# Kernel tuning notes

Measured on AMD Instinct MI355X. Metric: run time of the kernel, lower is better.

## Reference

```python
import jax, jax.numpy as jnp
import numpy as np

# NF4 codebook (QLoRA): 16 quantile values of a standard normal, normalized to [-1, 1]
NF4_TABLE = jnp.array([
    -1.0, -0.6961928009986877, -0.5250730514526367, -0.39491748809814453,
    -0.28444138169288635, -0.18477343022823334, -0.09105003625154495, 0.0,
    0.07958029955625534, 0.16093020141124725, 0.24611230194568634,
    0.33791524171829224, 0.44070982933044434, 0.5626170039176941,
    0.7229568362236328, 1.0], dtype=jnp.float32)

IN_DIM = 4096
OUT_DIM = 4096
RANK = 16
ALPHA = 32.0
BLOCK = 64  # NF4 quantization block size along the flattened weight


def setup_inputs() -> dict:
    key = jax.random.key(0)
    k1, k2, k3, k4, k5 = jax.random.split(key, 5)
    x = jax.random.normal(k1, (4, 2048, IN_DIM), dtype=jnp.float32)
    # 4-bit codes into NF4_TABLE, stored unpacked as int32
    w_codes = jax.random.randint(k2, (OUT_DIM, IN_DIM), 0, 16, dtype=jnp.int32)
    # per-block absmax scales (positive)
    w_scales = jax.random.uniform(k3, (OUT_DIM, IN_DIM // BLOCK), dtype=jnp.float32) * 0.02 + 1e-3
    # lora_a: kaiming-uniform-ish scale; lora_b: nonzero for testability (original inits to zeros)
    lora_a = jax.random.normal(k4, (RANK, IN_DIM), dtype=jnp.float32) * (1.0 / np.sqrt(IN_DIM))
    lora_b = jax.random.normal(k5, (OUT_DIM, RANK), dtype=jnp.float32) * 0.01
    return {"x": x, "w_codes": w_codes, "w_scales": w_scales, "lora_a": lora_a, "lora_b": lora_b}


def _dequant_nf4(w_codes, w_scales):
    # codes [O, I] -> dequantized weight [O, I]
    w = NF4_TABLE[w_codes]                                   # [O, I]
    w = w.reshape(OUT_DIM, IN_DIM // BLOCK, BLOCK) * w_scales[:, :, None]
    return w.reshape(OUT_DIM, IN_DIM)


def reference(x, w_codes, w_scales, lora_a, lora_b):
    # base: frozen NF4 linear (dequantize then matmul), no bias
    w = _dequant_nf4(w_codes, w_scales)                      # [O, I]
    base = jnp.einsum('bsi,oi->bso', x, w)                   # [B, S, O]
    # LoRA path: dropout p=0.0 -> identity; scale alpha / rank
    ax = jnp.einsum('bsi,ri->bsr', x, lora_a)                # [B, S, r]
    lora = jnp.einsum('bsr,or->bso', ax, lora_b)             # [B, S, O]
    return base + (ALPHA / RANK) * lora
```

## Files before the change

### kernel.cpp

```cpp
#include <hip/hip_runtime.h>
#include <hip/hip_bf16.h>


#define IN_DIM  4096
#define OUT_DIM 4096
#define RANK    16
#define M_TOK   8192
#define LORA_SCALE 2.0f

typedef __bf16 bf16_t;
typedef bf16_t bf16x8 __attribute__((ext_vector_type(8)));
typedef float  f32x4  __attribute__((ext_vector_type(4)));

__device__ __constant__ float NF4_TAB[16] = {
    -1.0f, -0.6961928009986877f, -0.5250730514526367f, -0.39491748809814453f,
    -0.28444138169288635f, -0.18477343022823334f, -0.09105003625154495f, 0.0f,
    0.07958029955625534f, 0.16093020141124725f, 0.24611230194568634f,
    0.33791524171829224f, 0.44070982933044434f, 0.5626170039176941f,
    0.7229568362236328f, 1.0f};

__global__ __launch_bounds__(256) void prep_w(
    const int* __restrict__ codes,
    const float* __restrict__ scales,
    const float* __restrict__ la,
    const float* __restrict__ lb,
    bf16_t* __restrict__ W)
{
    __shared__ float nf4s[16];
    __shared__ float lbs[16];
    const int o = blockIdx.x;
    const int tid = threadIdx.x;
    if (tid < 16) {
        nf4s[tid] = NF4_TAB[tid];
        lbs[tid]  = lb[o * RANK + tid] * LORA_SCALE;
    }
    __syncthreads();

    #pragma unroll
    for (int it = 0; it < 2; ++it) {
        const int i0 = (it * 256 + tid) * 8;
        const size_t base = (size_t)o * IN_DIM + i0;
        int4 c0 = *(const int4*)(codes + base);
        int4 c1 = *(const int4*)(codes + base + 4);
        const float sc = scales[o * (IN_DIM / 64) + (i0 >> 6)];
        float w[8];
        w[0] = nf4s[c0.x] * sc; w[1] = nf4s[c0.y] * sc;
        w[2] = nf4s[c0.z] * sc; w[3] = nf4s[c0.w] * sc;
        w[4] = nf4s[c1.x] * sc; w[5] = nf4s[c1.y] * sc;
        w[6] = nf4s[c1.z] * sc; w[7] = nf4s[c1.w] * sc;
        #pragma unroll
        for (int r = 0; r < RANK; ++r) {
            const float b = lbs[r];
            float4 a0 = *(const float4*)(la + r * IN_DIM + i0);
            float4 a1 = *(const float4*)(la + r * IN_DIM + i0 + 4);
            w[0] += b * a0.x; w[1] += b * a0.y; w[2] += b * a0.z; w[3] += b * a0.w;
            w[4] += b * a1.x; w[5] += b * a1.y; w[6] += b * a1.z; w[7] += b * a1.w;
        }
        bf16x8 v;
        #pragma unroll
        for (int j = 0; j < 8; ++j) v[j] = (bf16_t)w[j];
        *(bf16x8*)(W + base) = v;
    }
}

__global__ __launch_bounds__(256) void cast_x(
    const float* __restrict__ x, bf16_t* __restrict__ y, int n8)
{
    const int stride = gridDim.x * blockDim.x;
    for (int i = blockIdx.x * blockDim.x + threadIdx.x; i < n8; i += stride) {
        const size_t e = (size_t)i * 8;
        float4 a = *(const float4*)(x + e);
        float4 b = *(const float4*)(x + e + 4);
        bf16x8 v;
        v[0] = (bf16_t)a.x; v[1] = (bf16_t)a.y; v[2] = (bf16_t)a.z; v[3] = (bf16_t)a.w;
        v[4] = (bf16_t)b.x; v[5] = (bf16_t)b.y; v[6] = (bf16_t)b.z; v[7] = (bf16_t)b.w;
        *(bf16x8*)(y + e) = v;
    }
}

#define BM 256
#define BN 256
#define BK 32
#define NT (IN_DIM / BK)

__global__ __launch_bounds__(512, 2) void gemm_bt(
    const bf16_t* __restrict__ A, const bf16_t* __restrict__ B,
    float* __restrict__ C)
{
    __shared__ bf16_t lds[3][2][BM * BK];

    const int tid  = threadIdx.x;
    const int wave = tid >> 6;
    const int lane = tid & 63;

    const int flat = blockIdx.y * gridDim.x + blockIdx.x;
    const int swz  = (flat & 7) * 64 + (flat >> 3);
    const int bx = swz & 15;
    const int by = swz >> 4;
    const int m0 = by * BM;
    const int n0 = bx * BN;

    const int wr = wave >> 2;
    const int wc = wave & 3;

    f32x4 acc[8][4];
    #pragma unroll
    for (int i = 0; i < 8; ++i)
        #pragma unroll
        for (int j = 0; j < 4; ++j) acc[i][j] = (f32x4)0.0f;

    const size_t KB = (size_t)IN_DIM * 2;

    int s_row[2], s_gc[2];
    #pragma unroll
    for (int p = 0; p < 2; ++p) {
        const int off = p * 8192 + tid * 16;
        s_row[p] = off >> 6;
        s_gc[p]  = ((off >> 4) & 3) ^ ((s_row[p] >> 1) & 3);
    }
    const char* gA = (const char*)A;
    const char* gB = (const char*)B;

    const int frow = lane & 15;
    const int fch  = lane >> 4;
    int offA[8], offB[4];
    #pragma unroll
    for (int i = 0; i < 8; ++i) {
        const int ra = wr * 128 + i * 16 + frow;
        offA[i] = ra * 64 + ((fch ^ ((ra >> 1) & 3)) << 4);
    }
    #pragma unroll
    for (int j = 0; j < 4; ++j) {
        const int rb = wc * 64 + j * 16 + frow;
        offB[j] = rb * 64 + ((fch ^ ((rb >> 1) & 3)) << 4);
    }

#define STAGE(tt, bidx) do {                                                   \
    const size_t kb_ = (size_t)(tt) * (BK * 2);                                \
    _Pragma("unroll")                                                          \
    for (int p = 0; p < 2; ++p) {                                              \
        const char* srcA = gA + (size_t)(m0 + s_row[p]) * KB + kb_ + (s_gc[p] << 4); \
        const char* srcB = gB + (size_t)(n0 + s_row[p]) * KB + kb_ + (s_gc[p] << 4); \
        char* dA = (char*)&lds[bidx][0][0] + p * 8192 + wave * 1024;           \
        char* dB = (char*)&lds[bidx][1][0] + p * 8192 + wave * 1024;           \
        __builtin_amdgcn_global_load_lds(                                      \
            (const __attribute__((address_space(1))) void*)srcA,               \
            (__attribute__((address_space(3))) void*)dA, 16, 0, 0);            \
        __builtin_amdgcn_global_load_lds(                                      \
            (const __attribute__((address_space(1))) void*)srcB,               \
            (__attribute__((address_space(3))) void*)dB, 16, 0, 0);            \
    }                                                                          \
} while (0)

#define COMPUTE(bidx) do {                                                     \
    const char* bA_ = (const char*)&lds[bidx][0][0];                           \
    const char* bB_ = (const char*)&lds[bidx][1][0];                           \
    bf16x8 af[8], bfr[4];                                                      \
    _Pragma("unroll")                                                          \
    for (int i = 0; i < 8; ++i) af[i] = *(const bf16x8*)(bA_ + offA[i]);       \
    _Pragma("unroll")                                                          \
    for (int j = 0; j < 4; ++j) bfr[j] = *(const bf16x8*)(bB_ + offB[j]);      \
    asm volatile("s_waitcnt lgkmcnt(0)" ::: "memory");                         \
    __builtin_amdgcn_s_barrier();                                              \
    __builtin_amdgcn_s_setprio(1);                                             \
    _Pragma("unroll")                                                          \
    for (int i = 0; i < 8; ++i)                                                \
        _Pragma("unroll")                                                      \
        for (int j = 0; j < 4; ++j)                                            \
            acc[i][j] = __builtin_amdgcn_mfma_f32_16x16x32_bf16(               \
                af[i], bfr[j], acc[i][j], 0, 0, 0);                            \
    __builtin_amdgcn_s_setprio(0);                                             \
} while (0)

    STAGE(0, 0);
    STAGE(1, 1);

    int cb = 0, sb = 2;
    for (int t = 0; t < NT - 2; ++t) {
        STAGE(t + 2, sb);
        asm volatile("s_waitcnt vmcnt(8)" ::: "memory");
        __builtin_amdgcn_s_barrier();
        COMPUTE(cb);
        cb = (cb == 2) ? 0 : cb + 1;
        sb = (sb == 2) ? 0 : sb + 1;
    }
    asm volatile("s_waitcnt vmcnt(4)" ::: "memory");
    __builtin_amdgcn_s_barrier();
    COMPUTE(cb);
    cb = (cb == 2) ? 0 : cb + 1;
    asm volatile("s_waitcnt vmcnt(0)" ::: "memory");
    __builtin_amdgcn_s_barrier();
    COMPUTE(cb);

    const int crow = (lane >> 4) * 4;
    const int ccol = lane & 15;
    #pragma unroll
    for (int i = 0; i < 8; ++i) {
        #pragma unroll
        for (int j = 0; j < 4; ++j) {
            const int mb = m0 + wr * 128 + i * 16 + crow;
            const int nb = n0 + wc * 64 + j * 16 + ccol;
            #pragma unroll
            for (int r = 0; r < 4; ++r)
                C[(size_t)(mb + r) * OUT_DIM + nb] = acc[i][j][r];
        }
    }
#undef STAGE
#undef COMPUTE
}

extern "C" void kernel_launch(void* const* d_in, const int* in_sizes, int n_in,
                              void* d_out, int out_size, void* d_ws, size_t ws_size,
                              hipStream_t stream) {
    const float* x      = (const float*)d_in[0];
    const int*   codes  = (const int*)d_in[1];
    const float* scales = (const float*)d_in[2];
    const float* la     = (const float*)d_in[3];
    const float* lb     = (const float*)d_in[4];
    float* out = (float*)d_out;

    bf16_t* W  = (bf16_t*)d_ws;
    bf16_t* xb = (bf16_t*)((char*)d_ws + (size_t)OUT_DIM * IN_DIM * 2);

    prep_w<<<OUT_DIM, 256, 0, stream>>>(codes, scales, la, lb, W);
    cast_x<<<2048, 256, 0, stream>>>(x, xb, (M_TOK * IN_DIM) / 8);

    dim3 grid(OUT_DIM / BN, M_TOK / BM);
    gemm_bt<<<grid, 512, 0, stream>>>(xb, W, out);
}
```

Measured before the change: 351.4 us.

## Software-pipeline LDS fragment reads with MFMA halves and batch prep_w rows

The GEMM mainloop moves from a 3-buffer to a 4-buffer LDS ring. It keeps two register sets of A/B fragments so the next tile's LDS reads are issued between two halves of the MFMA block, hiding LDS read latency behind matrix math. The prep kernel now handles four output rows per block, so each lora_a load is reused four times, and it launches a quarter as many blocks. The trade-offs are a larger LDS footprint, higher register pressure from the doubled fragment buffers, and more intricate barrier and wait ordering that must stay correct.

```diff
diff --git a/kernel.cpp b/kernel.cpp
--- a/kernel.cpp
+++ b/kernel.cpp
@@ -27,39 +27,48 @@
     bf16_t* __restrict__ W)
 {
     __shared__ float nf4s[16];
-    __shared__ float lbs[16];
-    const int o = blockIdx.x;
+    __shared__ float lbs[4][16];
+    const int o0 = blockIdx.x * 4;
     const int tid = threadIdx.x;
-    if (tid < 16) {
-        nf4s[tid] = NF4_TAB[tid];
-        lbs[tid]  = lb[o * RANK + tid] * LORA_SCALE;
-    }
+    if (tid < 64) lbs[tid >> 4][tid & 15] = lb[(o0 + (tid >> 4)) * RANK + (tid & 15)] * LORA_SCALE;
+    else if (tid < 80) nf4s[tid - 64] = NF4_TAB[tid - 64];
     __syncthreads();
 
     #pragma unroll
     for (int it = 0; it < 2; ++it) {
         const int i0 = (it * 256 + tid) * 8;
-        const size_t base = (size_t)o * IN_DIM + i0;
-        int4 c0 = *(const int4*)(codes + base);
-        int4 c1 = *(const int4*)(codes + base + 4);
-        const float sc = scales[o * (IN_DIM / 64) + (i0 >> 6)];
-        float w[8];
-        w[0] = nf4s[c0.x] * sc; w[1] = nf4s[c0.y] * sc;
-        w[2] = nf4s[c0.z] * sc; w[3] = nf4s[c0.w] * sc;
-        w[4] = nf4s[c1.x] * sc; w[5] = nf4s[c1.y] * sc;
-        w[6] = nf4s[c1.z] * sc; w[7] = nf4s[c1.w] * sc;
+        float w[4][8];
+        #pragma unroll
+        for (int oo = 0; oo < 4; ++oo) {
+            const size_t base = (size_t)(o0 + oo) * IN_DIM + i0;
+            int4 c0 = *(const int4*)(codes + base);
+            int4 c1 = *(const int4*)(codes + base + 4);
+            const float sc = scales[(o0 + oo) * (IN_DIM / 64) + (i0 >> 6)];
+            w[oo][0] = nf4s[c0.x] * sc; w[oo][1] = nf4s[c0.y] * sc;
+            w[oo][2] = nf4s[c0.z] * sc; w[oo][3] = nf4s[c0.w] * sc;
+            w[oo][4] = nf4s[c1.x] * sc; w[oo][5] = nf4s[c1.y] * sc;
+            w[oo][6] = nf4s[c1.z] * sc; w[oo][7] = nf4s[c1.w] * sc;
+        }
         #pragma unroll
         for (int r = 0; r < RANK; ++r) {
-            const float b = lbs[r];
             float4 a0 = *(const float4*)(la + r * IN_DIM + i0);
             float4 a1 = *(const float4*)(la + r * IN_DIM + i0 + 4);
-            w[0] += b * a0.x; w[1] += b * a0.y; w[2] += b * a0.z; w[3] += b * a0.w;
-            w[4] += b * a1.x; w[5] += b * a1.y; w[6] += b * a1.z; w[7] += b * a1.w;
-        }
-        bf16x8 v;
-        #pragma unroll
-        for (int j = 0; j < 8; ++j) v[j] = (bf16_t)w[j];
-        *(bf16x8*)(W + base) = v;
+            #pragma unroll
+            for (int oo = 0; oo < 4; ++oo) {
+                const float b = lbs[oo][r];
+                w[oo][0] += b * a0.x; w[oo][1] += b * a0.y;
+                w[oo][2] += b * a0.z; w[oo][3] += b * a0.w;
+                w[oo][4] += b * a1.x; w[oo][5] += b * a1.y;
+                w[oo][6] += b * a1.z; w[oo][7] += b * a1.w;
+            }
+        }
+        #pragma unroll
+        for (int oo = 0; oo < 4; ++oo) {
+            bf16x8 v;
+            #pragma unroll
+            for (int j = 0; j < 8; ++j) v[j] = (bf16_t)w[oo][j];
+            *(bf16x8*)(W + (size_t)(o0 + oo) * IN_DIM + i0) = v;
+        }
     }
 }
 
@@ -87,7 +96,7 @@
     const bf16_t* __restrict__ A, const bf16_t* __restrict__ B,
     float* __restrict__ C)
 {
-    __shared__ bf16_t lds[3][2][BM * BK];
+    __shared__ bf16_t lds[4][2][BM * BK];
 
     const int tid  = threadIdx.x;
     const int wave = tid >> 6;
@@ -134,6 +143,8 @@
         const int rb = wc * 64 + j * 16 + frow;
         offB[j] = rb * 64 + ((fch ^ ((rb >> 1) & 3)) << 4);
     }
+
+#define LD(bidx) ((const char*)&lds[bidx][0][0])
 
 #define STAGE(tt, bidx) do {                                                   \
     const size_t kb_ = (size_t)(tt) * (BK * 2);                                \
@@ -152,45 +163,82 @@
     }                                                                          \
 } while (0)
 
-#define COMPUTE(bidx) do {                                                     \
-    const char* bA_ = (const char*)&lds[bidx][0][0];                           \
-    const char* bB_ = (const char*)&lds[bidx][1][0];                           \
-    bf16x8 af[8], bfr[4];                                                      \
-    _Pragma("unroll")                                                          \
-    for (int i = 0; i < 8; ++i) af[i] = *(const bf16x8*)(bA_ + offA[i]);       \
-    _Pragma("unroll")                                                          \
-    for (int j = 0; j < 4; ++j) bfr[j] = *(const bf16x8*)(bB_ + offB[j]);      \
+#define READ_FRAGS(AF, BF, base_) do {                                         \
+    const char* bA_ = (base_);                                                 \
+    const char* bB_ = (base_) + 16384;                                         \
+    _Pragma("unroll")                                                          \
+    for (int i = 0; i < 8; ++i) AF[i] = *(const bf16x8*)(bA_ + offA[i]);       \
+    _Pragma("unroll")                                                          \
+    for (int j = 0; j < 4; ++j) BF[j] = *(const bf16x8*)(bB_ + offB[j]);       \
+} while (0)
+
+#define WAIT_LGKM do {                                                         \
     asm volatile("s_waitcnt lgkmcnt(0)" ::: "memory");                         \
-    __builtin_amdgcn_s_barrier();                                              \
+    __builtin_amdgcn_sched_barrier(0);                                         \
+} while (0)
+
+#define MFMA_HALF(AF, BF, I0) do {                                             \
     __builtin_amdgcn_s_setprio(1);                                             \
     _Pragma("unroll")                                                          \
-    for (int i = 0; i < 8; ++i)                                                \
+    for (int i = 0; i < 4; ++i)                                                \
         _Pragma("unroll")                                                      \
         for (int j = 0; j < 4; ++j)                                            \
-            acc[i][j] = __builtin_amdgcn_mfma_f32_16x16x32_bf16(               \
-                af[i], bfr[j], acc[i][j], 0, 0, 0);                            \
+            acc[(I0) + i][j] = __builtin_amdgcn_mfma_f32_16x16x32_bf16(        \
+                AF[(I0) + i], BF[j], acc[(I0) + i][j], 0, 0, 0);               \
     __builtin_amdgcn_s_setprio(0);                                             \
 } while (0)
+
+    bf16x8 afE[8], bfE[4], afO[8], bfO[4];
 
     STAGE(0, 0);
     STAGE(1, 1);
-
-    int cb = 0, sb = 2;
-    for (int t = 0; t < NT - 2; ++t) {
-        STAGE(t + 2, sb);
+    STAGE(2, 2);
+    asm volatile("s_waitcnt vmcnt(8)" ::: "memory");
+    __builtin_amdgcn_s_barrier();
+    READ_FRAGS(afE, bfE, LD(0));
+
+    for (int t = 0; t < NT - 4; t += 2) {
+        STAGE(t + 3, (t + 3) & 3);
+        WAIT_LGKM;
+        MFMA_HALF(afE, bfE, 0);
         asm volatile("s_waitcnt vmcnt(8)" ::: "memory");
         __builtin_amdgcn_s_barrier();
-        COMPUTE(cb);
-        cb = (cb == 2) ? 0 : cb + 1;
-        sb = (sb == 2) ? 0 : sb + 1;
-    }
+        READ_FRAGS(afO, bfO, LD((t + 1) & 3));
+        MFMA_HALF(afE, bfE, 4);
+        STAGE(t + 4, (t + 4) & 3);
+        WAIT_LGKM;
+        MFMA_HALF(afO, bfO, 0);
+        asm volatile("s_waitcnt vmcnt(8)" ::: "memory");
+        __builtin_amdgcn_s_barrier();
+        READ_FRAGS(afE, bfE, LD((t + 2) & 3));
+        MFMA_HALF(afO, bfO, 4);
+    }
+
+    STAGE(127, 3);
+    WAIT_LGKM;
+    MFMA_HALF(afE, bfE, 0);
+    asm volatile("s_waitcnt vmcnt(8)" ::: "memory");
+    __builtin_amdgcn_s_barrier();
+    READ_FRAGS(afO, bfO, LD(1));
+    MFMA_HALF(afE, bfE, 4);
+
+    WAIT_LGKM;
+    MFMA_HALF(afO, bfO, 0);
     asm volatile("s_waitcnt vmcnt(4)" ::: "memory");
     __builtin_amdgcn_s_barrier();
-    COMPUTE(cb);
-    cb = (cb == 2) ? 0 : cb + 1;
+    READ_FRAGS(afE, bfE, LD(2));
+    MFMA_HALF(afO, bfO, 4);
+
+    WAIT_LGKM;
+    MFMA_HALF(afE, bfE, 0);
     asm volatile("s_waitcnt vmcnt(0)" ::: "memory");
     __builtin_amdgcn_s_barrier();
-    COMPUTE(cb);
+    READ_FRAGS(afO, bfO, LD(3));
+    MFMA_HALF(afE, bfE, 4);
+
+    WAIT_LGKM;
+    MFMA_HALF(afO, bfO, 0);
+    MFMA_HALF(afO, bfO, 4);
 
     const int crow = (lane >> 4) * 4;
     const int ccol = lane & 15;
@@ -206,7 +254,10 @@
         }
     }
 #undef STAGE
-#undef COMPUTE
+#undef READ_FRAGS
+#undef WAIT_LGKM
+#undef MFMA_HALF
+#undef LD
 }
 
 extern "C" void kernel_launch(void* const* d_in, const int* in_sizes, int n_in,
@@ -222,7 +273,7 @@
     bf16_t* W  = (bf16_t*)d_ws;
     bf16_t* xb = (bf16_t*)((char*)d_ws + (size_t)OUT_DIM * IN_DIM * 2);
 
-    prep_w<<<OUT_DIM, 256, 0, stream>>>(codes, scales, la, lb, W);
+    prep_w<<<OUT_DIM / 4, 256, 0, stream>>>(codes, scales, la, lb, W);
     cast_x<<<2048, 256, 0, stream>>>(x, xb, (M_TOK * IN_DIM) / 8);
 
     dim3 grid(OUT_DIM / BN, M_TOK / BM);
```

Measured after the change: 288.1 us. -18.0%, faster.
